# Performance work log

Hardware: AMD Instinct MI355X
Metric: run time of the kernel (lower is better)

## Reference

```python
import jax, jax.numpy as jnp
import numpy as np

B, C, H, W = 32, 128, 64, 64
D = 256          # attn_unit_dim
FF = 512         # ffn latent dim (2.0 * 256, rounded to /16*16)
NL = 2           # n_attn_blocks
PH = PW = 2      # patch size
EPS = 1e-5


def _cf_ln(x, g, b):
    # channel-first LayerNorm over dim 1 (unbiased=False variance)
    m = jnp.mean(x, axis=1, keepdims=True)
    v = jnp.mean((x - m) ** 2, axis=1, keepdims=True)
    return (x - m) * jax.lax.rsqrt(v + EPS) * g.reshape(1, -1, 1, 1) + b.reshape(1, -1, 1, 1)


def _conv1x1(x, w, b=None):
    y = jnp.einsum('bcpq,dc->bdpq', x, w)
    return y if b is None else y + b.reshape(1, -1, 1, 1)


def _bn(x, g, b, m, v):
    # eval-mode BatchNorm2d with running stats
    return (x - m.reshape(1, -1, 1, 1)) * jax.lax.rsqrt(v.reshape(1, -1, 1, 1) + EPS) \
        * g.reshape(1, -1, 1, 1) + b.reshape(1, -1, 1, 1)


def setup_inputs() -> dict:
    key = jax.random.key(0)
    ks = iter(jax.random.split(key, 64))
    rn = lambda shape, s=0.02: jax.random.normal(next(ks), shape, jnp.float32) * s
    pv = lambda shape: 1.0 + 0.1 * jax.random.uniform(next(ks), shape, jnp.float32)
    return {
        'x': jax.random.normal(next(ks), (B, C, H, W), jnp.float32),
        # local_rep: depthwise 3x3 + BN + leaky_relu, then 1x1 -> D
        'dw_w': rn((C, 1, 3, 3), 0.1),
        'bn1_g': pv((C,)), 'bn1_b': rn((C,), 0.1),
        'bn1_m': rn((C,), 0.1), 'bn1_v': pv((C,)),
        'c1_w': rn((D, C)), 'c1_b': rn((D,), 0.01),
        # per-layer transformer params (stacked over NL)
        'ln1_g': pv((NL, D)), 'ln1_b': rn((NL, D), 0.1),
        'qkv_w': rn((NL, 1 + 2 * D, D)), 'qkv_b': rn((NL, 1 + 2 * D), 0.01),
        'out_w': rn((NL, D, D)), 'out_b': rn((NL, D), 0.01),
        'ln2_g': pv((NL, D)), 'ln2_b': rn((NL, D), 0.1),
        'f1_w': rn((NL, FF, D)), 'f1_b': rn((NL, FF), 0.01),
        'f2_w': rn((NL, D, FF)), 'f2_b': rn((NL, D), 0.01),
        'lnf_g': pv((D,)), 'lnf_b': rn((D,), 0.1),
        # conv_proj: 1x1 (no bias) + BN
        'proj_w': rn((C, D)),
        'bn2_g': pv((C,)), 'bn2_b': rn((C,), 0.1),
        'bn2_m': rn((C,), 0.1), 'bn2_v': pv((C,)),
    }


def reference(x, dw_w, bn1_g, bn1_b, bn1_m, bn1_v, c1_w, c1_b,
              ln1_g, ln1_b, qkv_w, qkv_b, out_w, out_b,
              ln2_g, ln2_b, f1_w, f1_b, f2_w, f2_b,
              lnf_g, lnf_b, proj_w, bn2_g, bn2_b, bn2_m, bn2_v):
    # local representation: depthwise 3x3 conv + BN + leaky_relu(0.1) + 1x1 conv
    y = jax.lax.conv_general_dilated(
        x, dw_w, window_strides=(1, 1), padding=[(1, 1), (1, 1)],
        dimension_numbers=('NCHW', 'OIHW', 'NCHW'), feature_group_count=C)
    y = _bn(y, bn1_g, bn1_b, bn1_m, bn1_v)
    y = jax.nn.leaky_relu(y, 0.1)
    y = _conv1x1(y, c1_w, c1_b)                       # [B, D, H, W]

    # unfold -> [B, D, P, N], P = PH*PW pixels/patch, N = patches
    nh, nw = H // PH, W // PW
    p = y.reshape(B, D, nh, PH, nw, PW).transpose(0, 1, 3, 5, 2, 4).reshape(B, D, PH * PW, nh * nw)

    # global representation: NL pre-norm linear-attention transformer blocks
    for l in range(NL):
        z = _cf_ln(p, ln1_g[l], ln1_b[l])
        qkv = _conv1x1(z, qkv_w[l], qkv_b[l])          # [B, 1+2D, P, N]
        q, k, v = qkv[:, :1], qkv[:, 1:1 + D], qkv[:, 1 + D:]
        scores = jax.nn.softmax(q, axis=-1)            # softmax over patches N
        ctx = jnp.sum(k * scores, axis=-1, keepdims=True)  # [B, D, P, 1]
        attn = _conv1x1(jax.nn.relu(v) * ctx, out_w[l], out_b[l])
        p = p + attn
        z = _cf_ln(p, ln2_g[l], ln2_b[l])
        h = jax.nn.leaky_relu(_conv1x1(z, f1_w[l], f1_b[l]), 0.1)
        p = p + _conv1x1(h, f2_w[l], f2_b[l])
    p = _cf_ln(p, lnf_g, lnf_b)

    # fold back -> [B, D, H, W]
    fm = p.reshape(B, D, PH, PW, nh, nw).transpose(0, 1, 4, 2, 5, 3).reshape(B, D, H, W)

    # conv_proj: 1x1 (no bias) + BN -> [B, C, H, W]
    fm = _conv1x1(fm, proj_w)
    fm = _bn(fm, bn2_g, bn2_b, bn2_m, bn2_v)
    return fm
```

## Files before the change

kernel.cpp:

```cpp
#include <hip/hip_runtime.h>


typedef short  bh8 __attribute__((ext_vector_type(8)));
typedef float  f4  __attribute__((ext_vector_type(4)));
typedef unsigned short us2 __attribute__((ext_vector_type(2)));
typedef unsigned short us4 __attribute__((ext_vector_type(4)));

constexpr int Bc = 32, Cc = 128, Dc = 256, FFc = 512;
constexpr int NNc = 1024, Sc = 4096;
constexpr float EPSc = 1e-5f;

enum SrcMode { S_LNF32, S_BF16 };
enum OutMode { O_STOREF32, O_FOLDBN };

__device__ __forceinline__ unsigned short f2bf(float f) {
  union { float f; unsigned int u; } v; v.f = f;
  unsigned int u = v.u + 0x7FFFu + ((v.u >> 16) & 1u);
  return (unsigned short)(u >> 16);
}

__global__ __launch_bounds__(256) void k_wconv(
    const float* __restrict__ w, unsigned short* __restrict__ dst,
    int total, int klog2)
{
  int idx = blockIdx.x * 256 + threadIdx.x;
  if (idx >= total) return;
  int K = 1 << klog2;
  int m = idx >> klog2, k = idx & (K - 1);
  int Mt = total >> klog2;
  size_t a = ((size_t)((k >> 5) * (Mt >> 4) + (m >> 4)) * 64
              + (((k >> 3) & 3) << 4) + (m & 15)) * 8 + (k & 7);
  dst[a] = f2bf(w[idx]);
}

__global__ __launch_bounds__(256) void k_dwconv(
    const float* __restrict__ x, const float* __restrict__ dww,
    const float* __restrict__ g, const float* __restrict__ bb,
    const float* __restrict__ mm, const float* __restrict__ vv,
    unsigned short* __restrict__ y1)
{
  int idx = blockIdx.x * 256 + threadIdx.x;
  int w4 = (idx & 15) * 4;
  int h  = (idx >> 4) & 63;
  int c  = (idx >> 10) & 127;
  int bi = idx >> 17;
  const float* xb = x + (size_t)(bi * 128 + c) * Sc;
  const float* wp = dww + c * 9;
  float acc[4] = {0.f, 0.f, 0.f, 0.f};
  #pragma unroll
  for (int kh = 0; kh < 3; ++kh) {
    int rr = h + kh - 1;
    if (rr < 0 || rr > 63) continue;
    const float* row = xb + rr * 64;
    float4 m4 = *reinterpret_cast<const float4*>(row + w4);
    float v[6];
    v[0] = (w4 > 0)  ? row[w4 - 1] : 0.f;
    v[1] = m4.x; v[2] = m4.y; v[3] = m4.z; v[4] = m4.w;
    v[5] = (w4 < 60) ? row[w4 + 4] : 0.f;
    float w0 = wp[kh * 3], w1 = wp[kh * 3 + 1], w2 = wp[kh * 3 + 2];
    #pragma unroll
    for (int o = 0; o < 4; ++o)
      acc[o] += w0 * v[o] + w1 * v[o + 1] + w2 * v[o + 2];
  }
  float sc = g[c] * rsqrtf(vv[c] + EPSc);
  float sh = bb[c] - mm[c] * sc;
  unsigned short r[4];
  #pragma unroll
  for (int o = 0; o < 4; ++o) {
    float val = acc[o] * sc + sh;
    r[o] = f2bf(val > 0.f ? val : 0.1f * val);
  }
  int ph = h & 1;
  size_t base = (size_t)(bi * 128 + c) * Sc + (h >> 1) * 32 + (w4 >> 1);
  *reinterpret_cast<us2*>(y1 + base + (ph * 2 + 0) * NNc) = (us2){r[0], r[2]};
  *reinterpret_cast<us2*>(y1 + base + (ph * 2 + 1) * NNc) = (us2){r[1], r[3]};
}

template<bool QD>
__global__ __launch_bounds__(256) void k_lnstats(
    const float* __restrict__ p, const float* __restrict__ wgq,
    float* __restrict__ mean_, float* __restrict__ rstd_, float* __restrict__ qdot)
{
  __shared__ float wg_s[256];
  int t = threadIdx.x;
  if (QD) { wg_s[t] = wgq[t]; __syncthreads(); }
  int pos = blockIdx.x * 256 + t;
  int b = pos >> 12, s = pos & 4095;
  const float* base = p + (size_t)b * Dc * Sc + s;
  float sum = 0.f, sq = 0.f, qa = 0.f;
  for (int d = 0; d < Dc; ++d) {
    float v = base[(size_t)d * Sc];
    sum += v; sq += v * v;
    if (QD) qa += v * wg_s[d];
  }
  float m   = sum * (1.f / Dc);
  float var = sq * (1.f / Dc) - m * m;
  mean_[pos] = m;
  rstd_[pos] = rsqrtf(fmaxf(var, 0.f) + EPSc);
  if (QD) qdot[pos] = qa;
}

__global__ void k_prep(const float* __restrict__ wq, const float* __restrict__ lng,
                       const float* __restrict__ lnb, const float* __restrict__ qb,
                       float* __restrict__ wgq, float* __restrict__ scal)
{
  int t = threadIdx.x, lane = t & 63, wv = t >> 6;
  float w = wq[t];
  float a = w * lng[t], c2 = w * lnb[t];
  wgq[t] = a;
  __shared__ float ra[4], rb[4];
  #pragma unroll
  for (int off = 32; off > 0; off >>= 1) { a += __shfl_xor(a, off); c2 += __shfl_xor(c2, off); }
  if (lane == 0) { ra[wv] = a; rb[wv] = c2; }
  __syncthreads();
  if (t == 0) {
    scal[0] = ra[0] + ra[1] + ra[2] + ra[3];
    scal[1] = rb[0] + rb[1] + rb[2] + rb[3] + qb[0];
  }
}

__global__ __launch_bounds__(256) void k_softmax2(
    const float* __restrict__ qdot, const float* __restrict__ mean_,
    const float* __restrict__ rstd_, const float* __restrict__ scal,
    float* __restrict__ ub, float* __restrict__ Ub)
{
  int bp = blockIdx.x, b = bp >> 2, pp = bp & 3;
  int t = threadIdx.x, lane = t & 63, wv = t >> 6;
  __shared__ float r3[4], r4[4];
  float s1 = scal[0], s2 = scal[1];
  int pos0 = b * Sc + pp * NNc;
  float q[4], m_r[4], rs_r[4];
  float mx = -3.4e38f;
  #pragma unroll
  for (int i = 0; i < 4; ++i) {
    int pos = pos0 + t + i * 256;
    m_r[i] = mean_[pos]; rs_r[i] = rstd_[pos];
    q[i] = rs_r[i] * qdot[pos] - m_r[i] * rs_r[i] * s1 + s2;
    mx = fmaxf(mx, q[i]);
  }
  #pragma unroll
  for (int off = 32; off > 0; off >>= 1) mx = fmaxf(mx, __shfl_xor(mx, off));
  if (lane == 0) r3[wv] = mx;
  __syncthreads();
  mx = fmaxf(fmaxf(r3[0], r3[1]), fmaxf(r3[2], r3[3]));
  float sum = 0.f;
  #pragma unroll
  for (int i = 0; i < 4; ++i) { q[i] = __expf(q[i] - mx); sum += q[i]; }
  #pragma unroll
  for (int off = 32; off > 0; off >>= 1) sum += __shfl_xor(sum, off);
  if (lane == 0) r4[wv] = sum;
  __syncthreads();
  float inv = 1.f / (r4[0] + r4[1] + r4[2] + r4[3]);
  float pU = 0.f;
  #pragma unroll
  for (int i = 0; i < 4; ++i) {
    float un = rs_r[i] * q[i] * inv;
    ub[(size_t)bp * NNc + t + i * 256] = un;
    pU += m_r[i] * un;
  }
  #pragma unroll
  for (int off = 32; off > 0; off >>= 1) pU += __shfl_xor(pU, off);
  if (lane == 0) r3[wv] = pU;
  __syncthreads();
  if (t == 0) Ub[bp] = r3[0] + r3[1] + r3[2] + r3[3];
}

__global__ __launch_bounds__(256) void k_tpass(
    const float* __restrict__ p, const float* __restrict__ ub,
    const float* __restrict__ Ub, const float* __restrict__ lng,
    const float* __restrict__ lnb, float* __restrict__ tb)
{
  int cs = blockIdx.x, pp = blockIdx.y, b = blockIdx.z;
  int bp = b * 4 + pp;
  int t = threadIdx.x, lane = t & 63, wv = t >> 6;
  __shared__ float u_s[1024];
  for (int i = t; i < 1024; i += 256) u_s[i] = ub[(size_t)bp * NNc + i];
  __syncthreads();
  float U = Ub[bp];
  const float* pb = p + (size_t)b * Dc * Sc + pp * NNc;
  for (int i = 0; i < 16; ++i) {
    int c = cs * 64 + wv * 16 + i;
    const float* row = pb + (size_t)c * Sc;
    float sm = 0.f;
    #pragma unroll
    for (int j = 0; j < 16; ++j) { int n = lane + 64 * j; sm += row[n] * u_s[n]; }
    #pragma unroll
    for (int off = 32; off > 0; off >>= 1) sm += __shfl_xor(sm, off);
    if (lane == 0) tb[(size_t)bp * Dc + c] = lng[c] * (sm - U) + lnb[c];
  }
}

__global__ __launch_bounds__(256) void k_ctx2(
    const float* __restrict__ tb, const float* __restrict__ wk,
    const float* __restrict__ bk, float* __restrict__ ctxb)
{
  int b = blockIdx.x, d = threadIdx.x;
  __shared__ float ts[4][256];
  for (int i = threadIdx.x; i < 1024; i += 256) ts[i >> 8][i & 255] = tb[(size_t)b * 1024 + i];
  __syncthreads();
  const float* wrow = wk + (size_t)d * 256;
  float bkd = bk[d];
  float accp[4] = {0.f, 0.f, 0.f, 0.f};
  for (int c = 0; c < 256; c += 4) {
    float4 wv = *reinterpret_cast<const float4*>(wrow + c);
    #pragma unroll
    for (int pp = 0; pp < 4; ++pp)
      accp[pp] += wv.x * ts[pp][c] + wv.y * ts[pp][c + 1]
                + wv.z * ts[pp][c + 2] + wv.w * ts[pp][c + 3];
  }
  #pragma unroll
  for (int pp = 0; pp < 4; ++pp)
    ctxb[((size_t)(b * 256 + d)) * 4 + pp] = accp[pp] + bkd;
}

__global__ void k_bn2pre(const float* __restrict__ g, const float* __restrict__ bb,
                         const float* __restrict__ mm, const float* __restrict__ vv,
                         float* __restrict__ sc, float* __restrict__ sh)
{
  int c = threadIdx.x;
  if (c < Cc) {
    float s = g[c] * rsqrtf(vv[c] + EPSc);
    sc[c] = s;
    sh[c] = bb[c] - mm[c] * s;
  }
}

template<int M1, bool ATTN, bool QDOT>
__global__ __launch_bounds__(256) void k_fused(
    const float* __restrict__ p,
    const float* __restrict__ mean_, const float* __restrict__ rstd_,
    const float* __restrict__ lng, const float* __restrict__ lnb,
    const unsigned short* __restrict__ wf1, const float* __restrict__ b1,
    const float* __restrict__ ctxp,
    const unsigned short* __restrict__ wf2, const float* __restrict__ b2,
    float* __restrict__ dst,
    const float* __restrict__ wgq2,
    float* __restrict__ mean_o, float* __restrict__ rstd_o,
    float* __restrict__ qdot_o)
{
  constexpr int NT = 32;
  constexpr int NF = NT / 16;
  constexpr int ACC1 = M1 / 64;
  int t = threadIdx.x;
  int wv = t >> 6, lane = t & 63;
  int q = lane >> 4, ln16 = lane & 15;
  int nt = blockIdx.x, pp = blockIdx.y, b = blockIdx.z;
  int n0 = nt * NT;

  __shared__ unsigned int Alds[2][NT * 20];
  __shared__ unsigned short Frag[M1 * NT];
  __shared__ float m_s[NT], rs_s[NT];
  __shared__ float ctx_s[ATTN ? 256 : 4];

  int kp_s = t >> 4;
  int n2_s = (t & 15) * 2;

  size_t pbase = (size_t)b * Dc * Sc + pp * NNc + n0;

  float2 c0 = *reinterpret_cast<const float2*>(p + pbase + (size_t)(kp_s * 2) * Sc + n2_s);
  float2 c1 = *reinterpret_cast<const float2*>(p + pbase + (size_t)(kp_s * 2 + 1) * Sc + n2_s);

  if (t < NT) {
    int pos = b * Sc + pp * NNc + n0 + t;
    m_s[t]  = mean_[pos];
    rs_s[t] = rstd_[pos];
  }
  if (ATTN) ctx_s[t] = ctxp[(size_t)(b * Dc + t) * 4 + pp];

  f4 acc[ACC1][NF];
  #pragma unroll
  for (int i = 0; i < ACC1; ++i)
    #pragma unroll
    for (int j = 0; j < NF; ++j) acc[i][j] = (f4){0.f, 0.f, 0.f, 0.f};

  __syncthreads();

  for (int kc = 0; kc < 256; kc += 32) {
    int k0 = kc + kp_s * 2;
    float g0 = lng[k0], g1 = lng[k0 + 1];
    float h0 = lnb[k0], h1 = lnb[k0 + 1];
    float ms0 = m_s[n2_s],     rs0 = rs_s[n2_s];
    float ms1 = m_s[n2_s + 1], rs1 = rs_s[n2_s + 1];
    float a00 = (c0.x - ms0) * rs0 * g0 + h0;
    float a01 = (c0.y - ms1) * rs1 * g0 + h0;
    float a10 = (c1.x - ms0) * rs0 * g1 + h1;
    float a11 = (c1.y - ms1) * rs1 * g1 + h1;
    unsigned int pk0 = (unsigned int)f2bf(a00) | ((unsigned int)f2bf(a10) << 16);
    unsigned int pk1 = (unsigned int)f2bf(a01) | ((unsigned int)f2bf(a11) << 16);

    if (kc < 224) {
      c0 = *reinterpret_cast<const float2*>(p + pbase + (size_t)(kc + 32 + kp_s * 2) * Sc + n2_s);
      c1 = *reinterpret_cast<const float2*>(p + pbase + (size_t)(kc + 32 + kp_s * 2 + 1) * Sc + n2_s);
    }

    unsigned int* alw = Alds[(kc >> 5) & 1];
    alw[n2_s * 20 + kp_s]       = pk0;
    alw[(n2_s + 1) * 20 + kp_s] = pk1;

    bh8 aw[ACC1];
    #pragma unroll
    for (int tm = 0; tm < ACC1; ++tm)
      aw[tm] = *(const bh8*)(wf1 + ((size_t)((kc >> 5) * (M1 >> 4) + wv * ACC1 + tm) * 64 + lane) * 8);

    __syncthreads();

    const unsigned short* al = (const unsigned short*)Alds[(kc >> 5) & 1];
    #pragma unroll
    for (int tn = 0; tn < NF; ++tn) {
      bh8 bwf = *(const bh8*)(al + (tn * 16 + ln16) * 40 + q * 8);
      #pragma unroll
      for (int tm = 0; tm < ACC1; ++tm)
        acc[tm][tn] = __builtin_amdgcn_mfma_f32_16x16x32_bf16(aw[tm], bwf, acc[tm][tn], 0, 0, 0);
    }
  }

  #pragma unroll
  for (int tm = 0; tm < ACC1; ++tm) {
    int row0 = wv * (M1 / 4) + tm * 16 + q * 4;
    float bia[4], cxv[4];
    #pragma unroll
    for (int r = 0; r < 4; ++r) {
      bia[r] = b1[row0 + r];
      if (ATTN) cxv[r] = ctx_s[row0 + r];
    }
    int kt  = row0 >> 5;
    int sub = (row0 >> 3) & 3;
    int jo  = row0 & 7;
    #pragma unroll
    for (int tn = 0; tn < NF; ++tn) {
      int cl = tn * 16 + ln16;
      us4 pk;
      #pragma unroll
      for (int r = 0; r < 4; ++r) {
        float v = acc[tm][tn][r] + bia[r];
        if (ATTN) v = fmaxf(v, 0.f) * cxv[r];
        else      v = v > 0.f ? v : 0.1f * v;
        pk[r] = f2bf(v);
      }
      *reinterpret_cast<us4*>(Frag + (((kt * NF + (cl >> 4)) * 64 + (sub << 4 | (cl & 15))) * 8 + jo)) = pk;
    }
  }
  __syncthreads();

  f4 acc2[4][NF];
  #pragma unroll
  for (int i = 0; i < 4; ++i)
    #pragma unroll
    for (int j = 0; j < NF; ++j) acc2[i][j] = (f4){0.f, 0.f, 0.f, 0.f};

  for (int kc = 0; kc < M1; kc += 32) {
    bh8 aw2[4];
    #pragma unroll
    for (int tm = 0; tm < 4; ++tm)
      aw2[tm] = *(const bh8*)(wf2 + ((size_t)((kc >> 5) * 16 + wv * 4 + tm) * 64 + lane) * 8);
    #pragma unroll
    for (int tn = 0; tn < NF; ++tn) {
      bh8 bwf = *(const bh8*)(Frag + ((kc >> 5) * NF + tn) * 512 + lane * 8);
      #pragma unroll
      for (int tm = 0; tm < 4; ++tm)
        acc2[tm][tn] = __builtin_amdgcn_mfma_f32_16x16x32_bf16(aw2[tm], bwf, acc2[tm][tn], 0, 0, 0);
    }
  }

  float s1[NF], s2[NF], s3[NF];
  #pragma unroll
  for (int tn = 0; tn < NF; ++tn) { s1[tn] = 0.f; s2[tn] = 0.f; s3[tn] = 0.f; }
  #pragma unroll
  for (int tm = 0; tm < 4; ++tm) {
    #pragma unroll
    for (int r = 0; r < 4; ++r) {
      int row = wv * 64 + tm * 16 + q * 4 + r;
      float bv = b2[row];
      float wqr = QDOT ? wgq2[row] : 0.f;
      #pragma unroll
      for (int tn = 0; tn < NF; ++tn) {
        int col = n0 + tn * 16 + ln16;
        size_t da = (size_t)(b * Dc + row) * Sc + pp * NNc + col;
        float v = dst[da] + acc2[tm][tn][r] + bv;
        dst[da] = v;
        s1[tn] += v; s2[tn] += v * v;
        if (QDOT) s3[tn] += v * wqr;
      }
    }
  }
  #pragma unroll
  for (int tn = 0; tn < NF; ++tn) {
    s1[tn] += __shfl_xor(s1[tn], 16); s1[tn] += __shfl_xor(s1[tn], 32);
    s2[tn] += __shfl_xor(s2[tn], 16); s2[tn] += __shfl_xor(s2[tn], 32);
    if (QDOT) { s3[tn] += __shfl_xor(s3[tn], 16); s3[tn] += __shfl_xor(s3[tn], 32); }
  }
  __syncthreads();
  float* fr = (float*)Frag;
  if (q == 0) {
    #pragma unroll
    for (int tn = 0; tn < NF; ++tn) {
      int col = tn * 16 + ln16;
      fr[(wv * 3 + 0) * NT + col] = s1[tn];
      fr[(wv * 3 + 1) * NT + col] = s2[tn];
      fr[(wv * 3 + 2) * NT + col] = s3[tn];
    }
  }
  __syncthreads();
  if (t < NT) {
    float a1 = 0.f, a2 = 0.f, a3 = 0.f;
    #pragma unroll
    for (int w2 = 0; w2 < 4; ++w2) {
      a1 += fr[(w2 * 3 + 0) * NT + t];
      a2 += fr[(w2 * 3 + 1) * NT + t];
      a3 += fr[(w2 * 3 + 2) * NT + t];
    }
    int pos = b * Sc + pp * NNc + n0 + t;
    float mn  = a1 * (1.f / 256.f);
    float var = a2 * (1.f / 256.f) - mn * mn;
    mean_o[pos] = mn;
    rstd_o[pos] = rsqrtf(fmaxf(var, 0.f) + EPSc);
    if (QDOT) qdot_o[pos] = a3;
  }
}

template<int KTOT, int MTOT, int SRCCH, int SSTR, bool SPP,
         SrcMode SM, OutMode OM>
__global__ __launch_bounds__(256) void k_mm(
    const void* __restrict__ src,
    const float* __restrict__ mean_, const float* __restrict__ rstd_,
    const float* __restrict__ lng, const float* __restrict__ lnb,
    const unsigned short* __restrict__ wf, const float* __restrict__ bias,
    const float* __restrict__ bnsc, const float* __restrict__ bnsh,
    void* __restrict__ dst)
{
  int t = threadIdx.x;
  int wv = t >> 6, lane = t & 63;
  int wm = wv & 1, wn = wv >> 1;
  int q = lane >> 4, ln16 = lane & 15;
  int nb = blockIdx.x, b = blockIdx.z;
  int pp = blockIdx.y & 3, mb = blockIdx.y >> 2;
  int n0  = nb * 128;
  int MB0 = mb * 128;

  __shared__ unsigned int Alds[128 * 20];
  __shared__ float m_s[128], rs_s[128];

  if (SM == S_LNF32 && t < 128) {
    int pos = b * Sc + pp * NNc + n0 + t;
    m_s[t]  = mean_[pos];
    rs_s[t] = rstd_[pos];
  }

  f4 acc[4][4];
  #pragma unroll
  for (int i = 0; i < 4; ++i)
    #pragma unroll
    for (int j = 0; j < 4; ++j) acc[i][j] = (f4){0.f, 0.f, 0.f, 0.f};

  size_t sbase = (size_t)b * SRCCH * SSTR + pp * NNc + n0;
  int mtb = (MB0 >> 4) + wm * 4;

  for (int kc = 0; kc < KTOT; kc += 32) {
    bh8 aw[4];
    #pragma unroll
    for (int tm = 0; tm < 4; ++tm)
      aw[tm] = *(const bh8*)(wf + ((size_t)((kc >> 5) * (MTOT >> 4) + mtb + tm) * 64 + lane) * 8);
    __syncthreads();
    #pragma unroll
    for (int it = 0; it < 8; ++it) {
      int n_l = (t & 63) + (it & 1) * 64;
      int kp  = (t >> 6) + (it >> 1) * 4;
      int k0  = kc + kp * 2;
      unsigned int pk;
      if (SM == S_LNF32) {
        const float* sp = (const float*)src;
        float a0 = sp[sbase + (size_t)k0 * SSTR + n_l];
        float a1 = sp[sbase + (size_t)(k0 + 1) * SSTR + n_l];
        float ms = m_s[n_l], rs = rs_s[n_l];
        a0 = (a0 - ms) * rs * lng[k0] + lnb[k0];
        a1 = (a1 - ms) * rs * lng[k0 + 1] + lnb[k0 + 1];
        pk = (unsigned int)f2bf(a0) | ((unsigned int)f2bf(a1) << 16);
      } else {
        const unsigned short* sp = (const unsigned short*)src;
        unsigned int u0 = sp[sbase + (size_t)k0 * SSTR + n_l];
        unsigned int u1 = sp[sbase + (size_t)(k0 + 1) * SSTR + n_l];
        pk = u0 | (u1 << 16);
      }
      Alds[n_l * 20 + kp] = pk;
    }
    __syncthreads();
    const unsigned short* al = (const unsigned short*)Alds;
    #pragma unroll
    for (int tn = 0; tn < 4; ++tn) {
      int nrow = wn * 64 + tn * 16 + ln16;
      bh8 bwf = *(const bh8*)(al + nrow * 40 + q * 8);
      #pragma unroll
      for (int tm = 0; tm < 4; ++tm)
        acc[tm][tn] = __builtin_amdgcn_mfma_f32_16x16x32_bf16(aw[tm], bwf, acc[tm][tn], 0, 0, 0);
    }
  }

  #pragma unroll
  for (int tm = 0; tm < 4; ++tm) {
    #pragma unroll
    for (int r = 0; r < 4; ++r) {
      int row = MB0 + wm * 64 + tm * 16 + q * 4 + r;
      float scv = 0.f, shv = 0.f, bv = 0.f;
      if (OM == O_FOLDBN) { scv = bnsc[row]; shv = bnsh[row]; }
      else                { bv = bias[row]; }
      #pragma unroll
      for (int tn = 0; tn < 4; ++tn) {
        int col = n0 + wn * 64 + tn * 16 + ln16;
        float v = acc[tm][tn][r];
        if (OM == O_FOLDBN) {
          int hh = 2 * (col >> 5) + (pp >> 1), ww = 2 * (col & 31) + (pp & 1);
          ((float*)dst)[((size_t)(b * Cc + row)) * Sc + hh * 64 + ww] = v * scv + shv;
        } else {
          ((float*)dst)[(size_t)(b * MTOT + row) * Sc + pp * NNc + col] = v + bv;
        }
      }
    }
  }
}

extern "C" void kernel_launch(void* const* d_in, const int* in_sizes, int n_in,
                              void* d_out, int out_size, void* d_ws, size_t ws_size,
                              hipStream_t stream)
{
  const float* x     = (const float*)d_in[0];
  const float* dw_w  = (const float*)d_in[1];
  const float* bn1_g = (const float*)d_in[2];
  const float* bn1_b = (const float*)d_in[3];
  const float* bn1_m = (const float*)d_in[4];
  const float* bn1_v = (const float*)d_in[5];
  const float* c1_w  = (const float*)d_in[6];
  const float* c1_b  = (const float*)d_in[7];
  const float* ln1_g = (const float*)d_in[8];
  const float* ln1_b = (const float*)d_in[9];
  const float* qkv_w = (const float*)d_in[10];
  const float* qkv_b = (const float*)d_in[11];
  const float* out_w = (const float*)d_in[12];
  const float* out_b = (const float*)d_in[13];
  const float* ln2_g = (const float*)d_in[14];
  const float* ln2_b = (const float*)d_in[15];
  const float* f1_w  = (const float*)d_in[16];
  const float* f1_b  = (const float*)d_in[17];
  const float* f2_w  = (const float*)d_in[18];
  const float* f2_b  = (const float*)d_in[19];
  const float* lnf_g = (const float*)d_in[20];
  const float* lnf_b = (const float*)d_in[21];
  const float* projw = (const float*)d_in[22];
  const float* bn2_g = (const float*)d_in[23];
  const float* bn2_b = (const float*)d_in[24];
  const float* bn2_m = (const float*)d_in[25];
  const float* bn2_v = (const float*)d_in[26];
  float* out = (float*)d_out;

  float* ws    = (float*)d_ws;
  float* p     = ws;
  float* reg   = p + (size_t)33554432;
  unsigned short* y1u = (unsigned short*)reg;
  float* mean2 = reg;
  float* rstd2 = reg + 131072;
  float* meanb = reg   + (size_t)8388608;
  float* rstdb = meanb + 131072;
  float* qdotb = rstdb + 131072;
  float* ub    = qdotb + 131072;
  float* Ub    = ub    + 131072;
  float* tb    = Ub    + 128;
  float* ctxb  = tb    + 32768;
  float* wgq   = ctxb  + 32768;
  float* scal  = wgq   + 512;
  float* bnscb = scal  + 16;
  float* bnshb = bnscb + 128;
  unsigned short* wfb = (unsigned short*)(bnshb + 128);
  unsigned short* wf_c1   = wfb;
  unsigned short* wf_v0   = wfb + 32768;
  unsigned short* wf_proj = wfb + 32768 + 2 * 393216;

  k_wconv<<<128, 256, 0, stream>>>(c1_w, wf_c1, 256 * 128, 7);
  for (int l = 0; l < 2; ++l) {
    const float* wvp = qkv_w + ((size_t)l * 513 + 257) * Dc;
    unsigned short* base = wf_v0 + (size_t)l * 393216;
    k_wconv<<<256, 256, 0, stream>>>(wvp, base, 256 * 256, 8);
    k_wconv<<<256, 256, 0, stream>>>(out_w + (size_t)l * Dc * Dc, base + 65536, 256 * 256, 8);
    k_wconv<<<512, 256, 0, stream>>>(f1_w + (size_t)l * FFc * Dc, base + 131072, 512 * 256, 8);
    k_wconv<<<512, 256, 0, stream>>>(f2_w + (size_t)l * Dc * FFc, base + 262144, 256 * 512, 9);
  }
  k_wconv<<<128, 256, 0, stream>>>(projw, wf_proj, 128 * 256, 8);

  for (int l = 0; l < 2; ++l)
    k_prep<<<1, 256, 0, stream>>>(qkv_w + (size_t)l * 513 * Dc,
                                  ln1_g + l * Dc, ln1_b + l * Dc,
                                  qkv_b + l * 513, wgq + l * 256, scal + l * 2);

  k_dwconv<<<16384, 256, 0, stream>>>(x, dw_w, bn1_g, bn1_b, bn1_m, bn1_v, y1u);

  k_mm<128, 256, 128, 4096, true, S_BF16, O_STOREF32>
      <<<dim3(8, 8, 32), 256, 0, stream>>>(
      y1u, nullptr, nullptr, nullptr, nullptr, wf_c1, c1_b, nullptr, nullptr, p);

  k_lnstats<true><<<512, 256, 0, stream>>>(p, wgq, meanb, rstdb, qdotb);

  for (int l = 0; l < 2; ++l) {
    const float* g1 = ln1_g + l * Dc; const float* b1 = ln1_b + l * Dc;
    const float* g2 = ln2_g + l * Dc; const float* b2 = ln2_b + l * Dc;
    const float* wk = qkv_w + ((size_t)l * 513 + 1) * Dc;
    const float* bk = qkv_b + l * 513 + 1;
    const float* bvv = qkv_b + l * 513 + 257;
    unsigned short* wbase = wf_v0 + (size_t)l * 393216;

    k_softmax2<<<128, 256, 0, stream>>>(qdotb, meanb, rstdb, scal + l * 2, ub, Ub);
    k_tpass<<<dim3(4, 4, 32), 256, 0, stream>>>(p, ub, Ub, g1, b1, tb);
    k_ctx2<<<32, 256, 0, stream>>>(tb, wk, bk, ctxb);

    k_fused<256, true, false><<<dim3(32, 4, 32), 256, 0, stream>>>(
        p, meanb, rstdb, g1, b1, wbase, bvv, ctxb,
        wbase + 65536, out_b + l * Dc, p,
        nullptr, mean2, rstd2, nullptr);

    if (l == 0) {
      k_fused<512, false, true><<<dim3(32, 4, 32), 256, 0, stream>>>(
          p, mean2, rstd2, g2, b2, wbase + 131072, f1_b + l * FFc, nullptr,
          wbase + 262144, f2_b + l * Dc, p,
          wgq + 256, meanb, rstdb, qdotb);
    } else {
      k_fused<512, false, false><<<dim3(32, 4, 32), 256, 0, stream>>>(
          p, mean2, rstd2, g2, b2, wbase + 131072, f1_b + l * FFc, nullptr,
          wbase + 262144, f2_b + l * Dc, p,
          nullptr, meanb, rstdb, nullptr);
    }
  }

  k_bn2pre<<<1, 128, 0, stream>>>(bn2_g, bn2_b, bn2_m, bn2_v, bnscb, bnshb);
  k_mm<256, 128, 256, 4096, true, S_LNF32, O_FOLDBN>
      <<<dim3(8, 4, 32), 256, 0, stream>>>(
      p, meanb, rstdb, lnf_g, lnf_b, wf_proj, nullptr, bnscb, bnshb, out);
}
```

Before: 780.0 us.

## Split fused LN-GEMM-GEMM kernel across eight waves per block

The fused attention/FFN kernel now runs with 512 threads (8 waves) per block instead of 256, and each wave owns half as many output row tiles in both GEMM stages. The input staging is reworked so each thread loads single floats for one column rather than float2 for two, and the final row-statistics reduction sums over 8 wave partials. The aim is more resident waves and fewer accumulator registers per wave, to hide memory and MFMA latency better. In exchange there is an extra block barrier, narrower per-thread loads, and more waves competing for the same per-block weight fetches.

```diff
diff --git a/kernel.cpp b/kernel.cpp
--- a/kernel.cpp
+++ b/kernel.cpp
@@ -226,7 +226,7 @@
 }
 
 template<int M1, bool ATTN, bool QDOT>
-__global__ __launch_bounds__(256) void k_fused(
+__global__ __launch_bounds__(512, 2) void k_fused(
     const float* __restrict__ p,
     const float* __restrict__ mean_, const float* __restrict__ rstd_,
     const float* __restrict__ lng, const float* __restrict__ lnb,
@@ -239,8 +239,8 @@
     float* __restrict__ qdot_o)
 {
   constexpr int NT = 32;
-  constexpr int NF = NT / 16;
-  constexpr int ACC1 = M1 / 64;
+  constexpr int NF = 2;
+  constexpr int ACC1 = M1 / 128;
   int t = threadIdx.x;
   int wv = t >> 6, lane = t & 63;
   int q = lane >> 4, ln16 = lane & 15;
@@ -252,20 +252,20 @@
   __shared__ float m_s[NT], rs_s[NT];
   __shared__ float ctx_s[ATTN ? 256 : 4];
 
-  int kp_s = t >> 4;
-  int n2_s = (t & 15) * 2;
+  int kp_s = t >> 5;
+  int col  = t & 31;
 
   size_t pbase = (size_t)b * Dc * Sc + pp * NNc + n0;
 
-  float2 c0 = *reinterpret_cast<const float2*>(p + pbase + (size_t)(kp_s * 2) * Sc + n2_s);
-  float2 c1 = *reinterpret_cast<const float2*>(p + pbase + (size_t)(kp_s * 2 + 1) * Sc + n2_s);
+  float c0 = p[pbase + (size_t)(kp_s * 2) * Sc + col];
+  float c1 = p[pbase + (size_t)(kp_s * 2 + 1) * Sc + col];
 
   if (t < NT) {
     int pos = b * Sc + pp * NNc + n0 + t;
     m_s[t]  = mean_[pos];
     rs_s[t] = rstd_[pos];
   }
-  if (ATTN) ctx_s[t] = ctxp[(size_t)(b * Dc + t) * 4 + pp];
+  if (ATTN && t < 256) ctx_s[t] = ctxp[(size_t)(b * Dc + t) * 4 + pp];
 
   f4 acc[ACC1][NF];
   #pragma unroll
@@ -279,23 +279,17 @@
     int k0 = kc + kp_s * 2;
     float g0 = lng[k0], g1 = lng[k0 + 1];
     float h0 = lnb[k0], h1 = lnb[k0 + 1];
-    float ms0 = m_s[n2_s],     rs0 = rs_s[n2_s];
-    float ms1 = m_s[n2_s + 1], rs1 = rs_s[n2_s + 1];
-    float a00 = (c0.x - ms0) * rs0 * g0 + h0;
-    float a01 = (c0.y - ms1) * rs1 * g0 + h0;
-    float a10 = (c1.x - ms0) * rs0 * g1 + h1;
-    float a11 = (c1.y - ms1) * rs1 * g1 + h1;
-    unsigned int pk0 = (unsigned int)f2bf(a00) | ((unsigned int)f2bf(a10) << 16);
-    unsigned int pk1 = (unsigned int)f2bf(a01) | ((unsigned int)f2bf(a11) << 16);
+    float ms = m_s[col], rs = rs_s[col];
+    float a0 = (c0 - ms) * rs * g0 + h0;
+    float a1 = (c1 - ms) * rs * g1 + h1;
+    unsigned int pk = (unsigned int)f2bf(a0) | ((unsigned int)f2bf(a1) << 16);
 
     if (kc < 224) {
-      c0 = *reinterpret_cast<const float2*>(p + pbase + (size_t)(kc + 32 + kp_s * 2) * Sc + n2_s);
-      c1 = *reinterpret_cast<const float2*>(p + pbase + (size_t)(kc + 32 + kp_s * 2 + 1) * Sc + n2_s);
-    }
-
-    unsigned int* alw = Alds[(kc >> 5) & 1];
-    alw[n2_s * 20 + kp_s]       = pk0;
-    alw[(n2_s + 1) * 20 + kp_s] = pk1;
+      c0 = p[pbase + (size_t)(kc + 32 + kp_s * 2) * Sc + col];
+      c1 = p[pbase + (size_t)(kc + 32 + kp_s * 2 + 1) * Sc + col];
+    }
+
+    Alds[(kc >> 5) & 1][col * 20 + kp_s] = pk;
 
     bh8 aw[ACC1];
     #pragma unroll
@@ -314,9 +308,10 @@
     }
   }
 
+  __syncthreads();
   #pragma unroll
   for (int tm = 0; tm < ACC1; ++tm) {
-    int row0 = wv * (M1 / 4) + tm * 16 + q * 4;
+    int row0 = wv * (M1 / 8) + tm * 16 + q * 4;
     float bia[4], cxv[4];
     #pragma unroll
     for (int r = 0; r < 4; ++r) {
@@ -337,27 +332,27 @@
         else      v = v > 0.f ? v : 0.1f * v;
         pk[r] = f2bf(v);
       }
-      *reinterpret_cast<us4*>(Frag + (((kt * NF + (cl >> 4)) * 64 + (sub << 4 | (cl & 15))) * 8 + jo)) = pk;
-    }
-  }
-  __syncthreads();
-
-  f4 acc2[4][NF];
-  #pragma unroll
-  for (int i = 0; i < 4; ++i)
+      *reinterpret_cast<us4*>(Frag + (((kt * NF + (cl >> 4)) * 64 + ((sub << 4) | (cl & 15))) * 8 + jo)) = pk;
+    }
+  }
+  __syncthreads();
+
+  f4 acc2[2][NF];
+  #pragma unroll
+  for (int i = 0; i < 2; ++i)
     #pragma unroll
     for (int j = 0; j < NF; ++j) acc2[i][j] = (f4){0.f, 0.f, 0.f, 0.f};
 
   for (int kc = 0; kc < M1; kc += 32) {
-    bh8 aw2[4];
-    #pragma unroll
-    for (int tm = 0; tm < 4; ++tm)
-      aw2[tm] = *(const bh8*)(wf2 + ((size_t)((kc >> 5) * 16 + wv * 4 + tm) * 64 + lane) * 8);
+    bh8 aw2[2];
+    #pragma unroll
+    for (int tm = 0; tm < 2; ++tm)
+      aw2[tm] = *(const bh8*)(wf2 + ((size_t)((kc >> 5) * 16 + wv * 2 + tm) * 64 + lane) * 8);
     #pragma unroll
     for (int tn = 0; tn < NF; ++tn) {
       bh8 bwf = *(const bh8*)(Frag + ((kc >> 5) * NF + tn) * 512 + lane * 8);
       #pragma unroll
-      for (int tm = 0; tm < 4; ++tm)
+      for (int tm = 0; tm < 2; ++tm)
         acc2[tm][tn] = __builtin_amdgcn_mfma_f32_16x16x32_bf16(aw2[tm], bwf, acc2[tm][tn], 0, 0, 0);
     }
   }
@@ -366,16 +361,16 @@
   #pragma unroll
   for (int tn = 0; tn < NF; ++tn) { s1[tn] = 0.f; s2[tn] = 0.f; s3[tn] = 0.f; }
   #pragma unroll
-  for (int tm = 0; tm < 4; ++tm) {
+  for (int tm = 0; tm < 2; ++tm) {
     #pragma unroll
     for (int r = 0; r < 4; ++r) {
-      int row = wv * 64 + tm * 16 + q * 4 + r;
+      int row = wv * 32 + tm * 16 + q * 4 + r;
       float bv = b2[row];
       float wqr = QDOT ? wgq2[row] : 0.f;
       #pragma unroll
       for (int tn = 0; tn < NF; ++tn) {
-        int col = n0 + tn * 16 + ln16;
-        size_t da = (size_t)(b * Dc + row) * Sc + pp * NNc + col;
+        int cx = n0 + tn * 16 + ln16;
+        size_t da = (size_t)(b * Dc + row) * Sc + pp * NNc + cx;
         float v = dst[da] + acc2[tm][tn][r] + bv;
         dst[da] = v;
         s1[tn] += v; s2[tn] += v * v;
@@ -394,27 +389,27 @@
   if (q == 0) {
     #pragma unroll
     for (int tn = 0; tn < NF; ++tn) {
-      int col = tn * 16 + ln16;
-      fr[(wv * 3 + 0) * NT + col] = s1[tn];
-      fr[(wv * 3 + 1) * NT + col] = s2[tn];
-      fr[(wv * 3 + 2) * NT + col] = s3[tn];
+      int cx = tn * 16 + ln16;
+      fr[(wv * 3 + 0) * NT + cx] = s1[tn];
+      fr[(wv * 3 + 1) * NT + cx] = s2[tn];
+      fr[(wv * 3 + 2) * NT + cx] = s3[tn];
     }
   }
   __syncthreads();
   if (t < NT) {
-    float a1 = 0.f, a2 = 0.f, a3 = 0.f;
-    #pragma unroll
-    for (int w2 = 0; w2 < 4; ++w2) {
-      a1 += fr[(w2 * 3 + 0) * NT + t];
-      a2 += fr[(w2 * 3 + 1) * NT + t];
-      a3 += fr[(w2 * 3 + 2) * NT + t];
+    float a1s = 0.f, a2s = 0.f, a3s = 0.f;
+    #pragma unroll
+    for (int w2 = 0; w2 < 8; ++w2) {
+      a1s += fr[(w2 * 3 + 0) * NT + t];
+      a2s += fr[(w2 * 3 + 1) * NT + t];
+      a3s += fr[(w2 * 3 + 2) * NT + t];
     }
     int pos = b * Sc + pp * NNc + n0 + t;
-    float mn  = a1 * (1.f / 256.f);
-    float var = a2 * (1.f / 256.f) - mn * mn;
+    float mn  = a1s * (1.f / 256.f);
+    float var = a2s * (1.f / 256.f) - mn * mn;
     mean_o[pos] = mn;
     rstd_o[pos] = rsqrtf(fmaxf(var, 0.f) + EPSc);
-    if (QDOT) qdot_o[pos] = a3;
+    if (QDOT) qdot_o[pos] = a3s;
   }
 }
 
@@ -609,18 +604,18 @@
     k_tpass<<<dim3(4, 4, 32), 256, 0, stream>>>(p, ub, Ub, g1, b1, tb);
     k_ctx2<<<32, 256, 0, stream>>>(tb, wk, bk, ctxb);
 
-    k_fused<256, true, false><<<dim3(32, 4, 32), 256, 0, stream>>>(
+    k_fused<256, true, false><<<dim3(32, 4, 32), 512, 0, stream>>>(
         p, meanb, rstdb, g1, b1, wbase, bvv, ctxb,
         wbase + 65536, out_b + l * Dc, p,
         nullptr, mean2, rstd2, nullptr);
 
     if (l == 0) {
-      k_fused<512, false, true><<<dim3(32, 4, 32), 256, 0, stream>>>(
+      k_fused<512, false, true><<<dim3(32, 4, 32), 512, 0, stream>>>(
           p, mean2, rstd2, g2, b2, wbase + 131072, f1_b + l * FFc, nullptr,
           wbase + 262144, f2_b + l * Dc, p,
           wgq + 256, meanb, rstdb, qdotb);
     } else {
-      k_fused<512, false, false><<<dim3(32, 4, 32), 256, 0, stream>>>(
+      k_fused<512, false, false><<<dim3(32, 4, 32), 512, 0, stream>>>(
           p, mean2, rstd2, g2, b2, wbase + 131072, f1_b + l * FFc, nullptr,
           wbase + 262144, f2_b + l * Dc, p,
           nullptr, meanb, rstdb, nullptr);
```

Measured after the change: 796.6 us. 2.1% more time.
